# Kernel tuning notes

Hardware: AMD Instinct MI355X
Metric: run time of the kernel (lower is better)

Reference implementation:

```python
import jax, jax.numpy as jnp
import numpy as np

EPS = 1e-5
GROUPS = 32

def group_norm(x, w, b):
    B, C, D, H, W = x.shape
    g = x.reshape(B, GROUPS, C // GROUPS, D, H, W)
    mean = g.mean(axis=(2, 3, 4, 5), keepdims=True)
    var = g.var(axis=(2, 3, 4, 5), keepdims=True)
    g = (g - mean) * jax.lax.rsqrt(var + EPS)
    g = g.reshape(B, C, D, H, W)
    return g * w[None, :, None, None, None] + b[None, :, None, None, None]

def setup_inputs() -> dict:
    key = jax.random.key(0)
    ks = jax.random.split(key, 6)
    C = 256
    B, D, H, W = 2, 16, 16, 16
    xavier = math_scale = (6.0 / (C + C)) ** 0.5
    def xav(k):
        return jax.random.uniform(k, (C, C), jnp.float32, -xavier, xavier)
    return {
        "x": jax.random.normal(ks[0], (B, C, D, H, W), jnp.float32),
        "gn_w": jnp.ones((C,), jnp.float32),
        "gn_b": jnp.zeros((C,), jnp.float32),
        "wq": xav(ks[1]), "bq": jnp.zeros((C,), jnp.float32),
        "wk": xav(ks[2]), "bk": jnp.zeros((C,), jnp.float32),
        "wv": xav(ks[3]), "bv": jnp.zeros((C,), jnp.float32),
        "wp": xav(ks[4]), "bp": jnp.zeros((C,), jnp.float32),
    }

def reference(x, gn_w, gn_b, wq, bq, wk, bk, wv, bv, wp, bp):
    B, C, D, H, W = x.shape
    h = group_norm(x, gn_w, gn_b)
    hf = h.reshape(B, C, -1)  # (B, C, N)
    # 1x1x1 conv == channel-wise linear: weight (out_c, in_c)
    q = jnp.einsum('oc,bcn->bon', wq, hf) + bq[None, :, None]
    k = jnp.einsum('oc,bcn->bon', wk, hf) + bk[None, :, None]
    v = jnp.einsum('oc,bcn->bon', wv, hf) + bv[None, :, None]
    scale = C ** (-0.5)
    attn = jnp.einsum('bcn,bcm->bnm', q, k) * scale  # (B, N, N)
    attn = jax.nn.softmax(attn, axis=-1)
    out = jnp.einsum('bnm,bcm->bcn', attn, v)  # (B, C, N)
    out = jnp.einsum('oc,bcn->bon', wp, out) + bp[None, :, None]
    return x + out.reshape(B, C, D, H, W)
```

## Files before the change

kernel.cpp:

```cpp
#include <hip/hip_runtime.h>

#define C_DIM 256
#define N_SP  4096
#define B_DIM 2
#define CPG   8
#define EPS_GN 1e-5f
#define CN ((size_t)C_DIM * N_SP)

typedef unsigned short ushort_t;
typedef unsigned int uint_t;
typedef __attribute__((ext_vector_type(4))) float f32x4;
typedef __attribute__((ext_vector_type(4))) unsigned int u32x4;
typedef __attribute__((ext_vector_type(8))) short bf16x8;

__device__ inline ushort_t f2bf(float f) {
  union { float f; unsigned u; } v; v.f = f;
  unsigned r = v.u + 0x7FFF + ((v.u >> 16) & 1);
  return (ushort_t)(r >> 16);
}
__device__ inline uint_t pkbf(float a, float b) {
  return (uint_t)f2bf(a) | ((uint_t)f2bf(b) << 16);
}
__device__ inline float bf2f(uint_t u) {
  union { uint_t u; float f; } v; v.u = u << 16; return v.f;
}

#define GLOAD16(src, dst) __builtin_amdgcn_global_load_lds( \
    (const __attribute__((address_space(1))) unsigned int*)(src), \
    (__attribute__((address_space(3))) unsigned int*)(dst), 16, 0, 0)

__global__ __launch_bounds__(256) void wcvt_kernel(const float* __restrict__ wq,
    const float* __restrict__ wk, const float* __restrict__ wv,
    const float* __restrict__ wp, ushort_t* __restrict__ o) {
  int gid = blockIdx.x * 256 + threadIdx.x;
  int i4 = gid * 4;
  const float* s = (i4 < 65536) ? wq : (i4 < 131072) ? wk : (i4 < 196608) ? wv : wp;
  int off = i4 & 65535;
  float4 v = *(const float4*)(s + off);
  uint2 p; p.x = pkbf(v.x, v.y); p.y = pkbf(v.z, v.w);
  *(uint2*)&o[i4] = p;
}

__global__ __launch_bounds__(256) void gn_stats(const float* __restrict__ x,
    float* __restrict__ part) {
  const int bg = blockIdx.x, sub = blockIdx.y;
  const float* xp = x + (size_t)bg * CPG * N_SP + (size_t)sub * (CPG * N_SP / 4);
  const int tid = threadIdx.x;
  float s = 0.f, ss = 0.f;
  for (int i = tid; i < CPG * N_SP / 4; i += 256) {
    float v = xp[i];
    s += v; ss += v * v;
  }
#pragma unroll
  for (int off = 32; off > 0; off >>= 1) {
    s  += __shfl_down(s, off);
    ss += __shfl_down(ss, off);
  }
  __shared__ float rs[4], rss[4];
  const int wv = tid >> 6, ln = tid & 63;
  if (ln == 0) { rs[wv] = s; rss[wv] = ss; }
  __syncthreads();
  if (tid == 0) {
    part[(bg * 4 + sub) * 2]     = rs[0] + rs[1] + rs[2] + rs[3];
    part[(bg * 4 + sub) * 2 + 1] = rss[0] + rss[1] + rss[2] + rss[3];
  }
}

__global__ __launch_bounds__(256) void gn_apply(const float* __restrict__ x,
    const float* __restrict__ part, const float* __restrict__ w,
    const float* __restrict__ bgn, ushort_t* __restrict__ hT) {
  const int bg = blockIdx.x;
  const int b = bg >> 5, g = bg & 31;
  const int n0 = blockIdx.y * 256;
  const int tid = threadIdx.x;
  float S = 0.f, SS = 0.f;
#pragma unroll
  for (int i = 0; i < 4; ++i) {
    S  += part[(bg * 4 + i) * 2];
    SS += part[(bg * 4 + i) * 2 + 1];
  }
  const float mean = S / (float)(CPG * N_SP);
  const float var  = SS / (float)(CPG * N_SP) - mean * mean;
  const float rstd = rsqrtf(var + EPS_GN);
  float sc[8], sh[8];
#pragma unroll
  for (int c = 0; c < 8; ++c) {
    sc[c] = w[g * 8 + c] * rstd;
    sh[c] = bgn[g * 8 + c] - mean * sc[c];
  }
  __shared__ float tile[8][256];
  const float* xp = x + ((size_t)b * C_DIM + (size_t)g * CPG) * N_SP;
  for (int i = tid; i < 8 * 256; i += 256) {
    int cc = i >> 8, n = i & 255;
    tile[cc][n] = xp[(size_t)cc * N_SP + n0 + n];
  }
  __syncthreads();
  u32x4 pk4;
#pragma unroll
  for (int p = 0; p < 4; ++p)
    pk4[p] = pkbf(tile[2 * p][tid] * sc[2 * p] + sh[2 * p],
                  tile[2 * p + 1][tid] * sc[2 * p + 1] + sh[2 * p + 1]);
  *(u32x4*)&hT[((size_t)b * N_SP + n0 + tid) * C_DIM + g * 8] = pk4;
}

template <int MODE>
__global__ __launch_bounds__(256) void mgemm(
    const ushort_t* __restrict__ A, const ushort_t* __restrict__ Bm,
    const float* __restrict__ biasA, const float* __restrict__ biasB,
    ushort_t* __restrict__ outB, float* __restrict__ outF,
    const float* __restrict__ R, int aStride, int bStride, int ldo,
    size_t obStride) {
  __shared__ __align__(16) ushort_t a_lds[128 * 64];
  __shared__ __align__(16) ushort_t b_lds[128 * 64];
  const int bz = blockIdx.z;
  const ushort_t* Ab = A + (size_t)bz * aStride;
  const ushort_t* Bb = Bm + (size_t)bz * bStride;
  const int bm = blockIdx.y * 128, bn = blockIdx.x * 128;
  const int tid = threadIdx.x, wv = tid >> 6, ln = tid & 63;
  const int lo = ln & 15, g = ln >> 4;
  const int wr = wv >> 1, wc = wv & 1;

  f32x4 acc[4][4];
#pragma unroll
  for (int i = 0; i < 4; ++i)
#pragma unroll
    for (int j = 0; j < 4; ++j) acc[i][j] = (f32x4)(0.f);

  float bcol[4];
  float brow = 0.f;
  if (MODE == 0) {
#pragma unroll
    for (int ct = 0; ct < 4; ++ct) {
      int col = bn + wc * 64 + ct * 16 + lo;
      bcol[ct] = (col < 256) ? biasA[col] : biasB[col - 256];
    }
  } else {
    brow = biasA[bm + wr * 64 + ln];
  }

  for (int k0 = 0; k0 < C_DIM; k0 += 64) {
#pragma unroll
    for (int i = 0; i < 4; ++i) {
      int r0 = wv * 32 + i * 8;
      int row = r0 + (ln >> 3);
      GLOAD16(Ab + (size_t)(bm + row) * C_DIM + k0 + (((ln & 7) ^ (row & 7)) << 3),
              &a_lds[r0 * 64]);
      GLOAD16(Bb + (size_t)(bn + row) * C_DIM + k0 + (((ln & 7) ^ (row & 7)) << 3),
              &b_lds[r0 * 64]);
    }
    __syncthreads();
    bf16x8 af[4][2], bfr[4][2];
#pragma unroll
    for (int rt = 0; rt < 4; ++rt)
#pragma unroll
      for (int ks = 0; ks < 2; ++ks) {
        int row = wr * 64 + rt * 16 + lo;
        af[rt][ks] = *(const bf16x8*)&a_lds[row * 64 + (((ks * 4 + g) ^ (row & 7)) << 3)];
      }
#pragma unroll
    for (int ct = 0; ct < 4; ++ct)
#pragma unroll
      for (int ks = 0; ks < 2; ++ks) {
        int col = wc * 64 + ct * 16 + lo;
        bfr[ct][ks] = *(const bf16x8*)&b_lds[col * 64 + (((ks * 4 + g) ^ (col & 7)) << 3)];
      }
    __builtin_amdgcn_s_setprio(1);
#pragma unroll
    for (int ks = 0; ks < 2; ++ks)
#pragma unroll
      for (int rt = 0; rt < 4; ++rt)
#pragma unroll
        for (int ct = 0; ct < 4; ++ct)
          acc[rt][ct] = __builtin_amdgcn_mfma_f32_16x16x32_bf16(af[rt][ks], bfr[ct][ks], acc[rt][ct], 0, 0, 0);
    __builtin_amdgcn_s_setprio(0);
    __syncthreads();
  }

  float* wbase = (wv < 2 ? (float*)a_lds : (float*)b_lds) + (wv & 1) * 2048;
  const int grow = bm + wr * 64 + ln;
#pragma unroll
  for (int p = 0; p < 2; ++p) {
#pragma unroll
    for (int rt = 0; rt < 4; ++rt)
#pragma unroll
      for (int cth = 0; cth < 2; ++cth) {
        int ct = 2 * p + cth;
#pragma unroll
        for (int r = 0; r < 4; ++r) {
          int lrow = rt * 16 + 4 * g + r;
          int lcol = cth * 16 + lo;
          float v = acc[rt][ct][r];
          if (MODE == 0) v += bcol[ct];
          wbase[lrow * 32 + (lcol ^ ((lrow & 7) << 2))] = v;
        }
      }
    f32x4 buf[8];
#pragma unroll
    for (int cb = 0; cb < 8; ++cb) {
      int off = (4 * cb) ^ ((ln & 7) << 2);
      buf[cb] = *(const f32x4*)&wbase[ln * 32 + off];
    }
    const size_t obase = (size_t)grow * ldo + bn + wc * 64 + p * 32;
    if (MODE == 2) {
      const float* Rb = R + (size_t)bz * CN + obase;
      float* ob = outF + (size_t)bz * CN + obase;
#pragma unroll
      for (int cb = 0; cb < 8; ++cb) {
        f32x4 t = buf[cb];
        f32x4 rv = *(const f32x4*)&Rb[4 * cb];
#pragma unroll
        for (int j = 0; j < 4; ++j) t[j] += brow + rv[j];
        *(f32x4*)&ob[4 * cb] = t;
      }
    } else {
      float badd = (MODE == 0) ? 0.f : brow;
      ushort_t* ob = outB + (size_t)bz * obStride + obase;
      uint_t wpk[16];
#pragma unroll
      for (int k = 0; k < 16; ++k)
        wpk[k] = pkbf(buf[k >> 1][(k & 1) * 2] + badd, buf[k >> 1][(k & 1) * 2 + 1] + badd);
#pragma unroll
      for (int sidx = 0; sidx < 4; ++sidx) {
        u32x4 t;
        t[0] = wpk[4 * sidx]; t[1] = wpk[4 * sidx + 1];
        t[2] = wpk[4 * sidx + 2]; t[3] = wpk[4 * sidx + 3];
        *(u32x4*)&ob[sidx * 8] = t;
      }
    }
    __syncthreads();
  }
}

__global__ __launch_bounds__(256) void attn_mfma(
    const ushort_t* __restrict__ qk, const ushort_t* __restrict__ vt,
    ushort_t* __restrict__ pO, float* __restrict__ pml) {
  __shared__ __align__(16) ushort_t k_lds[64 * 256];
  __shared__ __align__(16) ushort_t v_lds[256 * 64];
  __shared__ __align__(16) ushort_t p_lds[4][16 * 64];

  const int ksplit = blockIdx.y;
  const int b  = blockIdx.z;
  const int q0 = blockIdx.x * 64;
  const int tid = threadIdx.x;
  const int wv = tid >> 6;
  const int ln = tid & 63;
  const int lo = ln & 15;
  const int g  = ln >> 4;

  const ushort_t* qtb = qk + (size_t)b * N_SP * 512;
  const ushort_t* ktb = qtb + 256;
  const ushort_t* vtb = vt + (size_t)b * CN;

  bf16x8 qf[8];
  {
    const ushort_t* qp = qtb + (size_t)(q0 + wv * 16 + lo) * 512 + g * 8;
#pragma unroll
    for (int ks = 0; ks < 8; ++ks) qf[ks] = *(const bf16x8*)(qp + ks * 32);
  }

  f32x4 o_acc[16];
#pragma unroll
  for (int i = 0; i < 16; ++i) o_acc[i] = (f32x4)(0.f);
  float m_run = -1e30f, l_run = 0.f;

  for (int t = 0; t < 16; ++t) {
    const int k0 = ksplit * 1024 + t * 64;
#pragma unroll
    for (int i = 0; i < 8; ++i) {
      int m = wv * 16 + i * 2 + (ln >> 5);
      int sl = ln & 31;
      GLOAD16(ktb + (size_t)(k0 + m) * 512 + ((sl ^ (m & 7)) * 8),
              &k_lds[(wv * 16 + i * 2) * 256]);
    }
#pragma unroll
    for (int i = 0; i < 8; ++i) {
      int c = wv * 64 + i * 8 + (ln >> 3);
      int sl = ln & 7;
      GLOAD16(vtb + (size_t)c * N_SP + k0 + ((sl ^ (c & 7)) * 8),
              &v_lds[(wv * 64 + i * 8) * 64]);
    }
    __syncthreads();

    f32x4 sacc[4];
#pragma unroll
    for (int kt = 0; kt < 4; ++kt) sacc[kt] = (f32x4)(0.f);
    __builtin_amdgcn_s_setprio(1);
#pragma unroll
    for (int ks = 0; ks < 8; ++ks) {
#pragma unroll
      for (int kt = 0; kt < 4; ++kt) {
        int m = lo + 16 * kt;
        bf16x8 kf = *(const bf16x8*)&k_lds[(m * 256 + g * 8 + ks * 32) ^ ((m & 7) << 3)];
        sacc[kt] = __builtin_amdgcn_mfma_f32_16x16x32_bf16(kf, qf[ks], sacc[kt], 0, 0, 0);
      }
    }
    __builtin_amdgcn_s_setprio(0);

    const float scale = 0.0625f;
    float pm = fmaxf(fmaxf(sacc[0][0], sacc[0][1]), fmaxf(sacc[0][2], sacc[0][3]));
#pragma unroll
    for (int kt = 1; kt < 4; ++kt)
      pm = fmaxf(pm, fmaxf(fmaxf(sacc[kt][0], sacc[kt][1]),
                           fmaxf(sacc[kt][2], sacc[kt][3])));
    pm = fmaxf(pm, __shfl_xor(pm, 16));
    pm = fmaxf(pm, __shfl_xor(pm, 32));
    pm *= scale;
    float alpha = 1.f;
    if (!__all(pm <= m_run + 8.f)) {
      float mn = fmaxf(m_run, pm);
      alpha = __expf(m_run - mn);
      m_run = mn;
    }
    float rsum = 0.f;
#pragma unroll
    for (int kt = 0; kt < 4; ++kt)
#pragma unroll
      for (int r = 0; r < 4; ++r) {
        float e = __expf(sacc[kt][r] * scale - m_run);
        rsum += e;
        p_lds[wv][(lo * 64 + kt * 16 + 4 * g + r) ^ ((lo & 7) << 3)] = f2bf(e);
      }
    rsum += __shfl_xor(rsum, 16);
    rsum += __shfl_xor(rsum, 32);
    l_run = l_run * alpha + rsum;
    if (!__all(alpha == 1.f)) {
#pragma unroll
      for (int i = 0; i < 16; ++i) o_acc[i] *= alpha;
    }

    __builtin_amdgcn_s_setprio(1);
#pragma unroll
    for (int ks2 = 0; ks2 < 2; ++ks2) {
      bf16x8 pf = *(const bf16x8*)&p_lds[wv][(lo * 64 + g * 8 + ks2 * 32) ^ ((lo & 7) << 3)];
#pragma unroll
      for (int ot = 0; ot < 16; ++ot) {
        int c = ot * 16 + lo;
        bf16x8 vf = *(const bf16x8*)&v_lds[(c * 64 + g * 8 + ks2 * 32) ^ ((c & 7) << 3)];
        o_acc[ot] = __builtin_amdgcn_mfma_f32_16x16x32_bf16(vf, pf, o_acc[ot], 0, 0, 0);
      }
    }
    __builtin_amdgcn_s_setprio(0);
    __syncthreads();
  }

  uint_t* tbase = (uint_t*)&k_lds[0] + wv * 2048;
#pragma unroll
  for (int ot = 0; ot < 16; ++ot)
#pragma unroll
    for (int p2 = 0; p2 < 2; ++p2) {
      uint_t w32 = pkbf(o_acc[ot][2 * p2], o_acc[ot][2 * p2 + 1]);
      int word = ot * 8 + 2 * g + p2;
      tbase[lo * 128 + (word ^ ((lo & 7) << 2))] = w32;
    }
  {
    const int q = ln >> 2, quarter = ln & 3;
    const size_t row32 = (((size_t)(ksplit * B_DIM + b) * N_SP) + q0 + wv * 16 + q) * (C_DIM / 2);
    uint_t* pO32 = (uint_t*)pO;
#pragma unroll
    for (int cb = 0; cb < 8; ++cb) {
      int off = (quarter * 32 + 4 * cb) ^ ((q & 7) << 2);
      u32x4 tv = *(const u32x4*)&tbase[q * 128 + off];
      *(u32x4*)&pO32[row32 + quarter * 32 + 4 * cb] = tv;
    }
  }
  if (g == 0) {
    int qn = q0 + wv * 16 + lo;
    size_t mi = (((size_t)(ksplit * B_DIM + b) * N_SP) + qn) * 2;
    pml[mi] = m_run;
    pml[mi + 1] = l_run;
  }
}

__global__ __launch_bounds__(256) void merge_kernel(const ushort_t* __restrict__ pO,
    const float* __restrict__ pml, ushort_t* __restrict__ aoT) {
  const int b = blockIdx.y;
  const int n = blockIdx.x * 16 + (threadIdx.x >> 4);
  const int cg = threadIdx.x & 15;
  float mi[4], li[4];
#pragma unroll
  for (int i = 0; i < 4; ++i) {
    size_t o = (((size_t)(i * B_DIM + b) * N_SP) + n) * 2;
    mi[i] = pml[o]; li[i] = pml[o + 1];
  }
  float ms = fmaxf(fmaxf(mi[0], mi[1]), fmaxf(mi[2], mi[3]));
  float wsum = 0.f, wi[4];
#pragma unroll
  for (int i = 0; i < 4; ++i) { wi[i] = __expf(mi[i] - ms); wsum += wi[i] * li[i]; }
  float inv = 1.f / wsum;
  float acc[16] = {};
#pragma unroll
  for (int i = 0; i < 4; ++i) {
    const ushort_t* p = pO + (((size_t)(i * B_DIM + b) * N_SP) + n) * C_DIM + cg * 16;
    u32x4 a = *(const u32x4*)p;
    u32x4 c2 = *(const u32x4*)(p + 8);
#pragma unroll
    for (int j = 0; j < 4; ++j) {
      acc[2 * j]     += wi[i] * bf2f(a[j] & 0xffffu);
      acc[2 * j + 1] += wi[i] * bf2f(a[j] >> 16);
      acc[8 + 2 * j]     += wi[i] * bf2f(c2[j] & 0xffffu);
      acc[8 + 2 * j + 1] += wi[i] * bf2f(c2[j] >> 16);
    }
  }
  ushort_t* ob = aoT + ((size_t)b * N_SP + n) * C_DIM + cg * 16;
  u32x4 o0, o1;
#pragma unroll
  for (int k = 0; k < 4; ++k) o0[k] = pkbf(acc[2 * k] * inv, acc[2 * k + 1] * inv);
#pragma unroll
  for (int k = 0; k < 4; ++k) o1[k] = pkbf(acc[8 + 2 * k] * inv, acc[8 + 2 * k + 1] * inv);
  *(u32x4*)&ob[0] = o0;
  *(u32x4*)&ob[8] = o1;
}

extern "C" void kernel_launch(void* const* d_in, const int* in_sizes, int n_in,
                              void* d_out, int out_size, void* d_ws, size_t ws_size,
                              hipStream_t stream) {
  const float* x   = (const float*)d_in[0];
  const float* gnw = (const float*)d_in[1];
  const float* gnb = (const float*)d_in[2];
  const float* wq  = (const float*)d_in[3];
  const float* bq  = (const float*)d_in[4];
  const float* wk  = (const float*)d_in[5];
  const float* bk  = (const float*)d_in[6];
  const float* wv  = (const float*)d_in[7];
  const float* bv  = (const float*)d_in[8];
  const float* wp  = (const float*)d_in[9];
  const float* bp  = (const float*)d_in[10];
  float* out = (float*)d_out;

  char* w8 = (char*)d_ws;
  ushort_t* hT  = (ushort_t*)(w8);
  ushort_t* wb  = (ushort_t*)(w8 + (4u << 20));
  ushort_t* qkw = (ushort_t*)(w8 + (4u << 20) + (1u << 19));
  ushort_t* vN  = (ushort_t*)(w8 + (12u << 20) + (1u << 19));
  ushort_t* aoT = (ushort_t*)(w8 + (16u << 20) + (1u << 19));
  float*    pml = (float*)(w8 + (20u << 20) + (1u << 19));
  ushort_t* pO  = (ushort_t*)(w8 + (20u << 20) + (1u << 19) + (1u << 18));
  float*    gnp = (float*)(w8 + (36u << 20) + (1u << 19) + (1u << 18));

  ushort_t* wvb = wb + 131072;
  ushort_t* wpb = wb + 196608;

  wcvt_kernel<<<dim3(256), dim3(256), 0, stream>>>(wq, wk, wv, wp, wb);
  gn_stats<<<dim3(B_DIM * 32, 4), dim3(256), 0, stream>>>(x, gnp);
  gn_apply<<<dim3(B_DIM * 32, 16), dim3(256), 0, stream>>>(x, gnp, gnw, gnb, hT);

  mgemm<0><<<dim3(4, 32, B_DIM), dim3(256), 0, stream>>>(
      hT, wb, bq, bk, qkw, nullptr, nullptr, (int)CN, 0, 512, (size_t)N_SP * 512);
  mgemm<1><<<dim3(32, 2, B_DIM), dim3(256), 0, stream>>>(
      wvb, hT, bv, nullptr, vN, nullptr, nullptr, 0, (int)CN, N_SP, CN);

  attn_mfma<<<dim3(64, 4, B_DIM), dim3(256), 0, stream>>>(qkw, vN, pO, pml);
  merge_kernel<<<dim3(256, B_DIM), dim3(256), 0, stream>>>(pO, pml, aoT);

  mgemm<2><<<dim3(32, 2, B_DIM), dim3(256), 0, stream>>>(
      wpb, aoT, bp, nullptr, nullptr, out, x, 0, (int)CN, N_SP, CN);
}
```

Before: 145.9 us.

## Use 32x32 MFMA tiles with 128-query blocks and double-buffered K/V staging

Rewrites the attention kernel so each wave handles 32 queries using 32x32x16 bf16 MFMA instead of 16x16x32, doubling the query tile per block to 128. K/V tiles are double-buffered in LDS so the next tile's global-to-LDS loads are issued while the current tile is computed. The grid halves to 256 blocks, and launch bounds of one block per CU let the larger register footprint and roughly 146KB of LDS fit. The risks are lower occupancy, fewer blocks than ideal across the CUs, and a float-staged epilogue with heavier LDS traffic.

```diff
diff --git a/kernel.cpp b/kernel.cpp
--- a/kernel.cpp
+++ b/kernel.cpp
@@ -10,6 +10,7 @@
 typedef unsigned short ushort_t;
 typedef unsigned int uint_t;
 typedef __attribute__((ext_vector_type(4))) float f32x4;
+typedef __attribute__((ext_vector_type(16))) float f32x16;
 typedef __attribute__((ext_vector_type(4))) unsigned int u32x4;
 typedef __attribute__((ext_vector_type(8))) short bf16x8;
 
@@ -231,78 +232,90 @@
   }
 }
 
-__global__ __launch_bounds__(256) void attn_mfma(
+__device__ __forceinline__ void stage_kv(const ushort_t* __restrict__ ktb,
+    const ushort_t* __restrict__ vtb, int k0, ushort_t* kbuf, ushort_t* vbuf,
+    int wv, int ln) {
+#pragma unroll
+  for (int i = 0; i < 8; ++i) {
+    int m = wv * 16 + i * 2 + (ln >> 5);
+    int sl = ln & 31;
+    GLOAD16(ktb + (size_t)(k0 + m) * 512 + ((sl ^ (m & 7)) * 8),
+            kbuf + (wv * 16 + i * 2) * 256);
+  }
+#pragma unroll
+  for (int i = 0; i < 8; ++i) {
+    int c = wv * 64 + i * 8 + (ln >> 3);
+    int sl = ln & 7;
+    GLOAD16(vtb + (size_t)c * N_SP + k0 + ((sl ^ (c & 7)) * 8),
+            vbuf + (wv * 64 + i * 8) * 64);
+  }
+}
+
+__global__ __launch_bounds__(256, 1) void attn_mfma(
     const ushort_t* __restrict__ qk, const ushort_t* __restrict__ vt,
     ushort_t* __restrict__ pO, float* __restrict__ pml) {
-  __shared__ __align__(16) ushort_t k_lds[64 * 256];
-  __shared__ __align__(16) ushort_t v_lds[256 * 64];
-  __shared__ __align__(16) ushort_t p_lds[4][16 * 64];
+  __shared__ __align__(16) ushort_t lds_all[32768 + 32768 + 9216];
 
   const int ksplit = blockIdx.y;
   const int b  = blockIdx.z;
-  const int q0 = blockIdx.x * 64;
+  const int q0 = blockIdx.x * 128;
   const int tid = threadIdx.x;
   const int wv = tid >> 6;
   const int ln = tid & 63;
-  const int lo = ln & 15;
-  const int g  = ln >> 4;
+  const int lq = ln & 31;
+  const int lh = ln >> 5;
 
   const ushort_t* qtb = qk + (size_t)b * N_SP * 512;
   const ushort_t* ktb = qtb + 256;
   const ushort_t* vtb = vt + (size_t)b * CN;
-
-  bf16x8 qf[8];
+  ushort_t* p_base = lds_all + 65536 + wv * (32 * 72);
+
+  bf16x8 qf[16];
   {
-    const ushort_t* qp = qtb + (size_t)(q0 + wv * 16 + lo) * 512 + g * 8;
-#pragma unroll
-    for (int ks = 0; ks < 8; ++ks) qf[ks] = *(const bf16x8*)(qp + ks * 32);
-  }
-
-  f32x4 o_acc[16];
-#pragma unroll
-  for (int i = 0; i < 16; ++i) o_acc[i] = (f32x4)(0.f);
+    const ushort_t* qp = qtb + (size_t)(q0 + wv * 32 + lq) * 512 + lh * 8;
+#pragma unroll
+    for (int ks = 0; ks < 16; ++ks) qf[ks] = *(const bf16x8*)(qp + ks * 16);
+  }
+
+  f32x16 oac[8];
+#pragma unroll
+  for (int i = 0; i < 8; ++i) oac[i] = (f32x16)(0.f);
   float m_run = -1e30f, l_run = 0.f;
 
+  const int kbase = ksplit * 1024;
+  stage_kv(ktb, vtb, kbase, lds_all, lds_all + 32768, wv, ln);
+  __syncthreads();
+
   for (int t = 0; t < 16; ++t) {
-    const int k0 = ksplit * 1024 + t * 64;
-#pragma unroll
-    for (int i = 0; i < 8; ++i) {
-      int m = wv * 16 + i * 2 + (ln >> 5);
-      int sl = ln & 31;
-      GLOAD16(ktb + (size_t)(k0 + m) * 512 + ((sl ^ (m & 7)) * 8),
-              &k_lds[(wv * 16 + i * 2) * 256]);
-    }
-#pragma unroll
-    for (int i = 0; i < 8; ++i) {
-      int c = wv * 64 + i * 8 + (ln >> 3);
-      int sl = ln & 7;
-      GLOAD16(vtb + (size_t)c * N_SP + k0 + ((sl ^ (c & 7)) * 8),
-              &v_lds[(wv * 64 + i * 8) * 64]);
-    }
-    __syncthreads();
-
-    f32x4 sacc[4];
-#pragma unroll
-    for (int kt = 0; kt < 4; ++kt) sacc[kt] = (f32x4)(0.f);
+    const int cur = t & 1;
+    ushort_t* kb = lds_all + cur * 16384;
+    ushort_t* vb = lds_all + 32768 + cur * 16384;
+    if (t + 1 < 16)
+      stage_kv(ktb, vtb, kbase + (t + 1) * 64,
+               lds_all + (cur ^ 1) * 16384,
+               lds_all + 32768 + (cur ^ 1) * 16384, wv, ln);
+
+    f32x16 s0 = (f32x16)(0.f), s1 = (f32x16)(0.f);
     __builtin_amdgcn_s_setprio(1);
 #pragma unroll
-    for (int ks = 0; ks < 8; ++ks) {
-#pragma unroll
-      for (int kt = 0; kt < 4; ++kt) {
-        int m = lo + 16 * kt;
-        bf16x8 kf = *(const bf16x8*)&k_lds[(m * 256 + g * 8 + ks * 32) ^ ((m & 7) << 3)];
-        sacc[kt] = __builtin_amdgcn_mfma_f32_16x16x32_bf16(kf, qf[ks], sacc[kt], 0, 0, 0);
-      }
+    for (int ks = 0; ks < 16; ++ks) {
+      bf16x8 kf0 = *(const bf16x8*)&kb[(lq * 256 + ks * 16 + lh * 8) ^ ((lq & 7) << 3)];
+      s0 = __builtin_amdgcn_mfma_f32_32x32x16_bf16(kf0, qf[ks], s0, 0, 0, 0);
+      int m1 = 32 + lq;
+      bf16x8 kf1 = *(const bf16x8*)&kb[(m1 * 256 + ks * 16 + lh * 8) ^ ((m1 & 7) << 3)];
+      s1 = __builtin_amdgcn_mfma_f32_32x32x16_bf16(kf1, qf[ks], s1, 0, 0, 0);
     }
     __builtin_amdgcn_s_setprio(0);
 
     const float scale = 0.0625f;
-    float pm = fmaxf(fmaxf(sacc[0][0], sacc[0][1]), fmaxf(sacc[0][2], sacc[0][3]));
-#pragma unroll
-    for (int kt = 1; kt < 4; ++kt)
-      pm = fmaxf(pm, fmaxf(fmaxf(sacc[kt][0], sacc[kt][1]),
-                           fmaxf(sacc[kt][2], sacc[kt][3])));
-    pm = fmaxf(pm, __shfl_xor(pm, 16));
+    float mx[16];
+#pragma unroll
+    for (int r = 0; r < 16; ++r) mx[r] = fmaxf(s0[r], s1[r]);
+#pragma unroll
+    for (int r = 0; r < 8; ++r) mx[r] = fmaxf(mx[r], mx[r + 8]);
+#pragma unroll
+    for (int r = 0; r < 4; ++r) mx[r] = fmaxf(mx[r], mx[r + 4]);
+    float pm = fmaxf(fmaxf(mx[0], mx[1]), fmaxf(mx[2], mx[3]));
     pm = fmaxf(pm, __shfl_xor(pm, 32));
     pm *= scale;
     float alpha = 1.f;
@@ -311,60 +324,66 @@
       alpha = __expf(m_run - mn);
       m_run = mn;
     }
+    float es[16];
     float rsum = 0.f;
 #pragma unroll
-    for (int kt = 0; kt < 4; ++kt)
-#pragma unroll
-      for (int r = 0; r < 4; ++r) {
-        float e = __expf(sacc[kt][r] * scale - m_run);
-        rsum += e;
-        p_lds[wv][(lo * 64 + kt * 16 + 4 * g + r) ^ ((lo & 7) << 3)] = f2bf(e);
-      }
-    rsum += __shfl_xor(rsum, 16);
+    for (int r = 0; r < 16; ++r) {
+      int key = (r & 3) + 8 * (r >> 2) + 4 * lh;
+      float e0 = __expf(s0[r] * scale - m_run);
+      float e1 = __expf(s1[r] * scale - m_run);
+      p_base[lq * 72 + key]      = f2bf(e0);
+      p_base[lq * 72 + 32 + key] = f2bf(e1);
+      es[r] = e0 + e1;
+    }
+#pragma unroll
+    for (int r = 0; r < 8; ++r) es[r] += es[r + 8];
+#pragma unroll
+    for (int r = 0; r < 4; ++r) es[r] += es[r + 4];
+    rsum = (es[0] + es[1]) + (es[2] + es[3]);
     rsum += __shfl_xor(rsum, 32);
     l_run = l_run * alpha + rsum;
     if (!__all(alpha == 1.f)) {
 #pragma unroll
-      for (int i = 0; i < 16; ++i) o_acc[i] *= alpha;
+      for (int i = 0; i < 8; ++i) oac[i] *= alpha;
     }
 
     __builtin_amdgcn_s_setprio(1);
 #pragma unroll
-    for (int ks2 = 0; ks2 < 2; ++ks2) {
-      bf16x8 pf = *(const bf16x8*)&p_lds[wv][(lo * 64 + g * 8 + ks2 * 32) ^ ((lo & 7) << 3)];
-#pragma unroll
-      for (int ot = 0; ot < 16; ++ot) {
-        int c = ot * 16 + lo;
-        bf16x8 vf = *(const bf16x8*)&v_lds[(c * 64 + g * 8 + ks2 * 32) ^ ((c & 7) << 3)];
-        o_acc[ot] = __builtin_amdgcn_mfma_f32_16x16x32_bf16(vf, pf, o_acc[ot], 0, 0, 0);
+    for (int ks2 = 0; ks2 < 4; ++ks2) {
+      bf16x8 pf = *(const bf16x8*)&p_base[lq * 72 + ks2 * 16 + lh * 8];
+#pragma unroll
+      for (int ot = 0; ot < 8; ++ot) {
+        int c = ot * 32 + lq;
+        bf16x8 vf = *(const bf16x8*)&vb[(c * 64 + ks2 * 16 + lh * 8) ^ ((c & 7) << 3)];
+        oac[ot] = __builtin_amdgcn_mfma_f32_32x32x16_bf16(vf, pf, oac[ot], 0, 0, 0);
       }
     }
     __builtin_amdgcn_s_setprio(0);
     __syncthreads();
   }
 
-  uint_t* tbase = (uint_t*)&k_lds[0] + wv * 2048;
-#pragma unroll
-  for (int ot = 0; ot < 16; ++ot)
-#pragma unroll
-    for (int p2 = 0; p2 < 2; ++p2) {
-      uint_t w32 = pkbf(o_acc[ot][2 * p2], o_acc[ot][2 * p2 + 1]);
-      int word = ot * 8 + 2 * g + p2;
-      tbase[lo * 128 + (word ^ ((lo & 7) << 2))] = w32;
+  float* sb = (float*)lds_all + wv * 8192;
+#pragma unroll
+  for (int ot = 0; ot < 8; ++ot)
+#pragma unroll
+    for (int r = 0; r < 16; ++r) {
+      int cl = (r & 3) + 8 * (r >> 2) + 4 * lh;
+      int c = ot * 32 + cl;
+      sb[lq * 256 + (c ^ ((lq & 7) << 2))] = oac[ot][r];
     }
   {
-    const int q = ln >> 2, quarter = ln & 3;
-    const size_t row32 = (((size_t)(ksplit * B_DIM + b) * N_SP) + q0 + wv * 16 + q) * (C_DIM / 2);
+    const int q = ln >> 1, half = ln & 1;
+    const size_t row32 = (((size_t)(ksplit * B_DIM + b) * N_SP) + q0 + wv * 32 + q) * 128;
     uint_t* pO32 = (uint_t*)pO;
 #pragma unroll
-    for (int cb = 0; cb < 8; ++cb) {
-      int off = (quarter * 32 + 4 * cb) ^ ((q & 7) << 2);
-      u32x4 tv = *(const u32x4*)&tbase[q * 128 + off];
-      *(u32x4*)&pO32[row32 + quarter * 32 + 4 * cb] = tv;
-    }
-  }
-  if (g == 0) {
-    int qn = q0 + wv * 16 + lo;
+    for (int j = 0; j < 32; ++j) {
+      f32x4 v4 = *(const f32x4*)&sb[q * 256 + ((half * 128 + 4 * j) ^ ((q & 7) << 2))];
+      uint2 pk2; pk2.x = pkbf(v4[0], v4[1]); pk2.y = pkbf(v4[2], v4[3]);
+      *(uint2*)&pO32[row32 + half * 64 + 2 * j] = pk2;
+    }
+  }
+  if (ln < 32) {
+    int qn = q0 + wv * 32 + lq;
     size_t mi = (((size_t)(ksplit * B_DIM + b) * N_SP) + qn) * 2;
     pml[mi] = m_run;
     pml[mi + 1] = l_run;
@@ -449,7 +468,7 @@
   mgemm<1><<<dim3(32, 2, B_DIM), dim3(256), 0, stream>>>(
       wvb, hT, bv, nullptr, vN, nullptr, nullptr, 0, (int)CN, N_SP, CN);
 
-  attn_mfma<<<dim3(64, 4, B_DIM), dim3(256), 0, stream>>>(qkw, vN, pO, pml);
+  attn_mfma<<<dim3(32, 4, B_DIM), dim3(256), 0, stream>>>(qkw, vN, pO, pml);
   merge_kernel<<<dim3(256, B_DIM), dim3(256), 0, stream>>>(pO, pml, aoT);
 
   mgemm<2><<<dim3(32, 2, B_DIM), dim3(256), 0, stream>>>(
```

Result: faster. 125.1 us (-14.3%).
